# Kernel optimization log

Measured on AMD Instinct MI355X. Metric: run time of the kernel, lower is better.

The kernel has to match this reference:

```python
import jax, jax.numpy as jnp
import numpy as np

N_NODES = 50000
N_EDGES = 600000
N_GRAPHS = 500
NODES_PER_GRAPH = 100
D = 128


def gcn_conv(x, W, b, src, dst, norm, n_nodes):
    # x' = D^-1/2 (A+I) D^-1/2 (x @ W) + b   (PyG GCNConv, add_self_loops=True)
    xw = x @ W                                # [N, out]
    msg = xw[src] * norm[:, None]             # [E+N, out]
    out = jax.ops.segment_sum(msg, dst, num_segments=n_nodes)
    return out + b


def setup_inputs() -> dict:
    key = jax.random.key(0)
    ks = jax.random.split(key, 8)
    x = jax.random.normal(ks[0], (N_NODES, D), dtype=jnp.float32)
    edge_index = jax.random.randint(ks[1], (2, N_EDGES), 0, N_NODES, dtype=jnp.int64)
    # batch: 500 graphs of 100 nodes each
    batch = jnp.repeat(jnp.arange(N_GRAPHS, dtype=jnp.int64), NODES_PER_GRAPH)
    # exactly 2 neighbor nodes per graph (first two of each graph)
    pat = jnp.zeros((NODES_PER_GRAPH,), dtype=jnp.float32).at[:2].set(1.0)
    is_neighbor = jnp.tile(pat, N_GRAPHS)
    scale = 1.0 / np.sqrt(D)
    W1 = jax.random.normal(ks[2], (D, D), dtype=jnp.float32) * scale
    b1 = jnp.zeros((D,), dtype=jnp.float32)
    W2 = jax.random.normal(ks[3], (D, D), dtype=jnp.float32) * scale
    b2 = jnp.zeros((D,), dtype=jnp.float32)
    W3 = jax.random.normal(ks[4], (D, D), dtype=jnp.float32) * scale
    b3 = jnp.zeros((D,), dtype=jnp.float32)
    return {"x": x, "edge_index": edge_index, "is_neighbor": is_neighbor,
            "batch": batch, "W1": W1, "b1": b1, "W2": W2, "b2": b2,
            "W3": W3, "b3": b3}


def reference(x, edge_index, is_neighbor, batch, W1, b1, W2, b2, W3, b3):
    n = x.shape[0]
    loop = jnp.arange(n, dtype=edge_index.dtype)
    src = jnp.concatenate([edge_index[0], loop])   # self loops appended
    dst = jnp.concatenate([edge_index[1], loop])
    deg = jax.ops.segment_sum(jnp.ones_like(dst, dtype=x.dtype), dst, num_segments=n)
    dinv = jnp.where(deg > 0, jax.lax.rsqrt(deg), 0.0)
    norm = dinv[src] * dinv[dst]                   # [E+N]

    h = gcn_conv(x, W1, b1, src, dst, norm, n)
    h = jax.nn.relu(h)
    h = gcn_conv(h, W2, b2, src, dst, norm, n)
    h = jax.nn.relu(h)
    h = gcn_conv(h, W3, b3, src, dst, norm, n)

    h = h * is_neighbor[:, None]
    pooled = jax.ops.segment_sum(h, batch, num_segments=N_GRAPHS)
    return pooled / 2.0
```

## Files before the change

### kernel.cpp

```cpp
#include <hip/hip_runtime.h>
#include <hip/hip_fp16.h>
#include <type_traits>

#define D 128

typedef __attribute__((ext_vector_type(8))) _Float16 f16x8;
typedef __attribute__((ext_vector_type(4))) float f32x4;


__global__ void count_kernel(const int* __restrict__ src, const int* __restrict__ dst,
                             const float* __restrict__ is_n,
                             int* __restrict__ cnt, int* __restrict__ mark, int E) {
    int e = blockIdx.x * blockDim.x + threadIdx.x;
    if (e < E) {
        int d = dst[e];
        atomicAdd(&cnt[d], 1);
        if (is_n[d] != 0.f) mark[src[e]] = 1;
    }
}

__global__ __launch_bounds__(256) void psumB_kernel(const int* __restrict__ cnt,
                                                    const int* __restrict__ mark,
                                                    const float* __restrict__ is_n,
                                                    int* __restrict__ bsum_c,
                                                    int* __restrict__ bsum_m, int n) {
    __shared__ int s[256], s2[256];
    int t = threadIdx.x;
    int i = blockIdx.x * 256 + t;
    s[t] = (i < n) ? cnt[i] : 0;
    s2[t] = (i < n) ? (mark[i] | (is_n[i] != 0.f ? 1 : 0)) : 0;
    __syncthreads();
    for (int off = 128; off > 0; off >>= 1) {
        if (t < off) { s[t] += s[t + off]; s2[t] += s2[t + off]; }
        __syncthreads();
    }
    if (t == 0) { bsum_c[blockIdx.x] = s[0]; bsum_m[blockIdx.x] = s2[0]; }
}

__global__ __launch_bounds__(256) void bscanB_kernel(const int* __restrict__ bsum_c,
                                                     const int* __restrict__ bsum_m,
                                                     int* __restrict__ boff_c,
                                                     int* __restrict__ boff_m,
                                                     int* __restrict__ na, int PB) {
    __shared__ int s[256];
    int t = threadIdx.x;
    int v = (t < PB) ? bsum_c[t] : 0;
    s[t] = v;
    __syncthreads();
    for (int off = 1; off < 256; off <<= 1) {
        int add = (t >= off) ? s[t - off] : 0;
        __syncthreads();
        s[t] += add;
        __syncthreads();
    }
    if (t < PB) boff_c[t] = s[t] - v;
    __syncthreads();
    int v2 = (t < PB) ? bsum_m[t] : 0;
    s[t] = v2;
    __syncthreads();
    for (int off = 1; off < 256; off <<= 1) {
        int add = (t >= off) ? s[t - off] : 0;
        __syncthreads();
        s[t] += add;
        __syncthreads();
    }
    if (t < PB) boff_m[t] = s[t] - v2;
    if (t == PB - 1) na[0] = s[t];
}

__global__ __launch_bounds__(256) void finB_kernel(const int* __restrict__ cnt,
                                                   const int* __restrict__ mark,
                                                   const float* __restrict__ is_n,
                                                   const int* __restrict__ boff_c,
                                                   const int* __restrict__ boff_m,
                                                   int* __restrict__ rowstart,
                                                   int* __restrict__ cursor,
                                                   float* __restrict__ dinv,
                                                   int* __restrict__ act, int n, int E) {
    __shared__ int s[256];
    int t = threadIdx.x;
    int i = blockIdx.x * 256 + t;
    int c = (i < n) ? cnt[i] : 0;
    s[t] = c;
    __syncthreads();
    for (int off = 1; off < 256; off <<= 1) {
        int add = (t >= off) ? s[t - off] : 0;
        __syncthreads();
        s[t] += add;
        __syncthreads();
    }
    if (i < n) {
        int excl = s[t] - c + boff_c[blockIdx.x];
        rowstart[i] = excl;
        cursor[i] = excl;
        dinv[i] = rsqrtf(1.0f + (float)c);
    }
    if (i == 0) rowstart[n] = E;
    __syncthreads();
    int m = (i < n) ? (mark[i] | (is_n[i] != 0.f ? 1 : 0)) : 0;
    s[t] = m;
    __syncthreads();
    for (int off = 1; off < 256; off <<= 1) {
        int add = (t >= off) ? s[t - off] : 0;
        __syncthreads();
        s[t] += add;
        __syncthreads();
    }
    if (m) act[s[t] - 1 + boff_m[blockIdx.x]] = i;
}

__global__ void fill_kernel(const int* __restrict__ src, const int* __restrict__ dst,
                            int* __restrict__ cursor, int* __restrict__ csr_src, int E) {
    int e = blockIdx.x * blockDim.x + threadIdx.x;
    if (e < E) {
        int d = dst[e];
        int pos = atomicAdd(&cursor[d], 1);
        csr_src[pos] = src[e];
    }
}


__global__ __launch_bounds__(256) void packw_kernel(const float* __restrict__ W1,
                                                    const float* __restrict__ W2,
                                                    const float* __restrict__ W3,
                                                    __half* __restrict__ Wp) {
    int gid = blockIdx.x * 256 + threadIdx.x;
    int m = gid >> 11;
    int idx = gid & 2047;
    const float* W = (m == 0) ? W1 : (m == 1) ? W2 : W3;
    int l = idx & 63;
    int nt = (idx >> 6) & 7;
    int ks = idx >> 9;
    int kb = ks * 32 + (l >> 4) * 8;
    int col = nt * 16 + (l & 15);
    __half tmp[8];
#pragma unroll
    for (int j = 0; j < 8; j++) tmp[j] = __float2half(W[(kb + j) * D + col]);
    *(float4*)&Wp[(size_t)gid * 8] = *(float4*)tmp;
}


template <typename AT>
__global__ __launch_bounds__(256, 2) void gemm_mfma_kernel(const AT* __restrict__ X,
                                                           const __half* __restrict__ Wp,
                                                           const float* __restrict__ dinv,
                                                           __half* __restrict__ Y, int M) {
    int lane = threadIdx.x & 63;
    int wid = threadIdx.x >> 6;
    f16x8 bf[4][8];
    {
        const float4* wp = (const float4*)Wp;
#pragma unroll
        for (int ks = 0; ks < 4; ks++)
#pragma unroll
            for (int nt = 0; nt < 8; nt++) {
                float4 t = wp[(ks * 8 + nt) * 64 + lane];
                bf[ks][nt] = *(f16x8*)&t;
            }
    }
    int row_l = lane & 15;
    int kgrp = lane >> 4;
    int tiles = M >> 4;
    int nw = gridDim.x * 4;
    for (int tile = blockIdx.x * 4 + wid; tile < tiles; tile += nw) {
        int row0 = tile << 4;
        const AT* ap = X + (size_t)(row0 + row_l) * D + kgrp * 8;
        f32x4 acc[8];
#pragma unroll
        for (int nt = 0; nt < 8; nt++) acc[nt] = (f32x4){0.f, 0.f, 0.f, 0.f};
#pragma unroll
        for (int ks = 0; ks < 4; ks++) {
            f16x8 a;
            if constexpr (std::is_same<AT, float>::value) {
                float4 a0 = *(const float4*)(ap + ks * 32);
                float4 a1 = *(const float4*)(ap + ks * 32 + 4);
                a[0] = (_Float16)a0.x; a[1] = (_Float16)a0.y;
                a[2] = (_Float16)a0.z; a[3] = (_Float16)a0.w;
                a[4] = (_Float16)a1.x; a[5] = (_Float16)a1.y;
                a[6] = (_Float16)a1.z; a[7] = (_Float16)a1.w;
            } else {
                float4 t = *(const float4*)(const void*)(ap + ks * 32);
                a = *(f16x8*)&t;
            }
#pragma unroll
            for (int nt = 0; nt < 8; nt++)
                acc[nt] = __builtin_amdgcn_mfma_f32_16x16x32_f16(a, bf[ks][nt],
                                                                 acc[nt], 0, 0, 0);
        }
        float ds[4];
#pragma unroll
        for (int r = 0; r < 4; r++) ds[r] = dinv[row0 + kgrp * 4 + r];
        __half* yb = Y + (size_t)row0 * D;
#pragma unroll
        for (int nt = 0; nt < 8; nt++)
#pragma unroll
            for (int r = 0; r < 4; r++)
                yb[(size_t)(kgrp * 4 + r) * D + nt * 16 + row_l] =
                    __float2half(ds[r] * acc[nt][r]);
    }
}


__device__ __forceinline__ void add_row(float acc[8], const __half* __restrict__ XWs,
                                        int u, int l16) {
    float4 r = ((const float4*)(XWs + (size_t)u * D))[l16];
    const __half2* h2 = (const __half2*)&r;
#pragma unroll
    for (int k = 0; k < 4; k++) {
        float2 f = __half22float2(h2[k]);
        acc[2 * k]     += f.x;
        acc[2 * k + 1] += f.y;
    }
}

__device__ __forceinline__ void gather_grp(const __half* __restrict__ XWs,
                                           const int* __restrict__ csr_src,
                                           int v, int e0, int e1, int l16,
                                           float acc[8]) {
#pragma unroll
    for (int k = 0; k < 8; k++) acc[k] = 0.f;
    int j = e0;
    for (; j + 1 < e1; j += 2) {
        int u0 = csr_src[j];
        int u1 = csr_src[j + 1];
        float4 r0 = ((const float4*)(XWs + (size_t)u0 * D))[l16];
        float4 r1 = ((const float4*)(XWs + (size_t)u1 * D))[l16];
        const __half2* a0 = (const __half2*)&r0;
        const __half2* a1 = (const __half2*)&r1;
#pragma unroll
        for (int k = 0; k < 4; k++) {
            float2 f0 = __half22float2(a0[k]);
            float2 f1 = __half22float2(a1[k]);
            acc[2 * k]     += f0.x + f1.x;
            acc[2 * k + 1] += f0.y + f1.y;
        }
    }
    if (j < e1) add_row(acc, XWs, csr_src[j], l16);
    add_row(acc, XWs, v, l16);
}


__global__ __launch_bounds__(256) void agg_gemm_kernel(const __half* __restrict__ XWs,
                                                       const float* __restrict__ bias,
                                                       const float* __restrict__ dinv,
                                                       const int* __restrict__ rowstart,
                                                       const int* __restrict__ csr_src,
                                                       const __half* __restrict__ Wp2,
                                                       __half* __restrict__ Y) {
    __shared__ __half hs[16][136];
    int t = threadIdx.x;
    int wid = t >> 6, lane = t & 63;
    int g = lane >> 4, l16 = lane & 15;
    int block0 = blockIdx.x * 16;
    int v = block0 + wid * 4 + g;
    int e0 = rowstart[v], e1 = rowstart[v + 1];
    float acc[8];
    gather_grp(XWs, csr_src, v, e0, e1, l16, acc);
    float dv = dinv[v];
    float4 b0 = ((const float4*)bias)[l16 * 2];
    float4 b1 = ((const float4*)bias)[l16 * 2 + 1];
    __half o[8];
    o[0] = __float2half(fmaxf(b0.x + dv * acc[0], 0.f));
    o[1] = __float2half(fmaxf(b0.y + dv * acc[1], 0.f));
    o[2] = __float2half(fmaxf(b0.z + dv * acc[2], 0.f));
    o[3] = __float2half(fmaxf(b0.w + dv * acc[3], 0.f));
    o[4] = __float2half(fmaxf(b1.x + dv * acc[4], 0.f));
    o[5] = __float2half(fmaxf(b1.y + dv * acc[5], 0.f));
    o[6] = __float2half(fmaxf(b1.z + dv * acc[6], 0.f));
    o[7] = __float2half(fmaxf(b1.w + dv * acc[7], 0.f));
    *(float4*)&hs[wid * 4 + g][l16 * 8] = *(float4*)o;
    f16x8 bf[4][2];
    {
        const float4* wp = (const float4*)Wp2;
#pragma unroll
        for (int ks = 0; ks < 4; ks++)
#pragma unroll
            for (int j = 0; j < 2; j++) {
                float4 tmp = wp[(ks * 8 + wid * 2 + j) * 64 + lane];
                bf[ks][j] = *(f16x8*)&tmp;
            }
    }
    __syncthreads();
    int row_l = l16, kgrp = g;
    f32x4 acc2[2];
    acc2[0] = (f32x4){0.f, 0.f, 0.f, 0.f};
    acc2[1] = (f32x4){0.f, 0.f, 0.f, 0.f};
#pragma unroll
    for (int ks = 0; ks < 4; ks++) {
        f16x8 a = *(f16x8*)&hs[row_l][ks * 32 + kgrp * 8];
#pragma unroll
        for (int j = 0; j < 2; j++)
            acc2[j] = __builtin_amdgcn_mfma_f32_16x16x32_f16(a, bf[ks][j],
                                                             acc2[j], 0, 0, 0);
    }
    float ds[4];
#pragma unroll
    for (int r = 0; r < 4; r++) ds[r] = dinv[block0 + kgrp * 4 + r];
    __half* yb = Y + (size_t)block0 * D;
#pragma unroll
    for (int j = 0; j < 2; j++)
#pragma unroll
        for (int r = 0; r < 4; r++)
            yb[(size_t)(kgrp * 4 + r) * D + (wid * 2 + j) * 16 + row_l] =
                __float2half(ds[r] * acc2[j][r]);
}


__global__ __launch_bounds__(256) void agg_act_kernel(const __half* __restrict__ XWs,
                                                      const float* __restrict__ bias,
                                                      const float* __restrict__ dinv,
                                                      const int* __restrict__ rowstart,
                                                      const int* __restrict__ csr_src,
                                                      const int* __restrict__ act,
                                                      const int* __restrict__ na_p,
                                                      __half* __restrict__ out) {
    int t = threadIdx.x;
    int wid = t >> 6, lane = t & 63;
    int g = lane >> 4, l16 = lane & 15;
    int na = na_p[0];
    int stride = gridDim.x * 16;
    float4 b0 = ((const float4*)bias)[l16 * 2];
    float4 b1 = ((const float4*)bias)[l16 * 2 + 1];
    for (int i = blockIdx.x * 16 + wid * 4 + g; i < na; i += stride) {
        int v = act[i];
        int e0 = rowstart[v], e1 = rowstart[v + 1];
        float acc[8];
        gather_grp(XWs, csr_src, v, e0, e1, l16, acc);
        float dv = dinv[v];
        __half o[8];
        o[0] = __float2half(dv * fmaxf(b0.x + dv * acc[0], 0.f));
        o[1] = __float2half(dv * fmaxf(b0.y + dv * acc[1], 0.f));
        o[2] = __float2half(dv * fmaxf(b0.z + dv * acc[2], 0.f));
        o[3] = __float2half(dv * fmaxf(b0.w + dv * acc[3], 0.f));
        o[4] = __float2half(dv * fmaxf(b1.x + dv * acc[4], 0.f));
        o[5] = __float2half(dv * fmaxf(b1.y + dv * acc[5], 0.f));
        o[6] = __float2half(dv * fmaxf(b1.z + dv * acc[6], 0.f));
        o[7] = __float2half(dv * fmaxf(b1.w + dv * acc[7], 0.f));
        *(float4*)&out[(size_t)v * D + l16 * 8] = *(float4*)o;
    }
}


__global__ __launch_bounds__(256) void agg_pool_kernel(const __half* __restrict__ Hs,
                                                       const float* __restrict__ dinv,
                                                       const int* __restrict__ rowstart,
                                                       const int* __restrict__ csr_src,
                                                       const float* __restrict__ is_n,
                                                       const int* __restrict__ batch,
                                                       float* __restrict__ P,
                                                       float* __restrict__ cg, int n) {
    int t = threadIdx.x;
    int wid = t >> 6, lane = t & 63;
    int g = lane >> 4, l16 = lane & 15;
    int v = blockIdx.x * 16 + wid * 4 + g;
    float w_is = is_n[v];
    if (__ballot(w_is != 0.f) == 0ULL) return;
    if (w_is != 0.f) {
        int e0 = rowstart[v], e1 = rowstart[v + 1];
        float acc[8];
        gather_grp(Hs, csr_src, v, e0, e1, l16, acc);
        float s = w_is * dinv[v];
        int gr = batch[v];
        float* pb = &P[(size_t)gr * D + l16 * 8];
#pragma unroll
        for (int k = 0; k < 8; k++) atomicAdd(&pb[k], s * acc[k]);
        if (l16 == 0) atomicAdd(&cg[gr], w_is);
    }
}

__global__ __launch_bounds__(64) void pool_gemm_kernel(const float* __restrict__ P,
                                                       const float* __restrict__ cg,
                                                       const float* __restrict__ W,
                                                       const float* __restrict__ b,
                                                       float* __restrict__ out, int G) {
    int g = blockIdx.x;
    if (g >= G) return;
    int c = threadIdx.x * 2;
    float2 acc = {0.f, 0.f};
    const float* pr = &P[(size_t)g * D];
#pragma unroll 4
    for (int k = 0; k < D; k++) {
        float pk = pr[k];
        float2 w = *(const float2*)&W[k * D + c];
        acc.x += pk * w.x;
        acc.y += pk * w.y;
    }
    float s = 0.5f * cg[g];
    float2 bb = *(const float2*)&b[c];
    out[(size_t)g * D + c]     = 0.5f * acc.x + s * bb.x;
    out[(size_t)g * D + c + 1] = 0.5f * acc.y + s * bb.y;
}


extern "C" void kernel_launch(void* const* d_in, const int* in_sizes, int n_in,
                              void* d_out, int out_size, void* d_ws, size_t ws_size,
                              hipStream_t stream) {
    const float* x     = (const float*)d_in[0];
    const int*   edge  = (const int*)d_in[1];
    const float* is_n  = (const float*)d_in[2];
    const int*   batch = (const int*)d_in[3];
    const float* W1 = (const float*)d_in[4];
    const float* b1 = (const float*)d_in[5];
    const float* W2 = (const float*)d_in[6];
    const float* b2 = (const float*)d_in[7];
    const float* W3 = (const float*)d_in[8];
    const float* b3 = (const float*)d_in[9];
    float* out = (float*)d_out;

    int n = in_sizes[0] / D;
    int E = in_sizes[1] / 2;
    int G = out_size / D;
    const int* esrc = edge;
    const int* edst = edge + E;

    char* p = (char*)d_ws;
    __half* xw = (__half*)p;     p += (size_t)n * D * sizeof(float);
    __half* h  = (__half*)p;     p += (size_t)n * D * sizeof(float);
    float* dinv = (float*)p;     p += (size_t)n * sizeof(float);
    int* rowstart = (int*)p;     p += (size_t)(n + 1) * sizeof(int);
    int* cursor = (int*)p;       p += (size_t)n * sizeof(int);
    int* csr_src = (int*)p;      p += (size_t)E * sizeof(int);
    int* bsum_c = (int*)p;       p += 256 * sizeof(int);
    int* bsum_m = (int*)p;       p += 256 * sizeof(int);
    int* boff_c = (int*)p;       p += 256 * sizeof(int);
    int* boff_m = (int*)p;       p += 256 * sizeof(int);
    int* act = (int*)p;          p += (size_t)n * sizeof(int);
    int* na = (int*)p;           p += 4 * sizeof(int);
    __half* Wp = (__half*)p;     p += (size_t)3 * D * D * sizeof(__half);
    int* cnt = (int*)p;          p += (size_t)n * sizeof(int);
    int* mark = (int*)p;         p += (size_t)n * sizeof(int);
    float* P = (float*)p;        p += (size_t)G * D * sizeof(float);
    float* cg = (float*)p;       p += (size_t)G * sizeof(float);
    size_t zbytes = (size_t)(2 * n) * sizeof(int) + (size_t)(G * D + G) * sizeof(float);

    int PB = (n + 255) / 256;

    hipMemsetAsync(cnt, 0, zbytes, stream);
    packw_kernel<<<24, 256, 0, stream>>>(W1, W2, W3, Wp);
    count_kernel<<<(E + 255) / 256, 256, 0, stream>>>(esrc, edst, is_n, cnt, mark, E);
    psumB_kernel<<<PB, 256, 0, stream>>>(cnt, mark, is_n, bsum_c, bsum_m, n);
    bscanB_kernel<<<1, 256, 0, stream>>>(bsum_c, bsum_m, boff_c, boff_m, na, PB);
    finB_kernel<<<PB, 256, 0, stream>>>(cnt, mark, is_n, boff_c, boff_m,
                                        rowstart, cursor, dinv, act, n, E);
    fill_kernel<<<(E + 255) / 256, 256, 0, stream>>>(esrc, edst, cursor, csr_src, E);

    gemm_mfma_kernel<float><<<512, 256, 0, stream>>>(x, Wp, dinv, xw, n);
    agg_gemm_kernel<<<n / 16, 256, 0, stream>>>(xw, b1, dinv, rowstart, csr_src,
                                                Wp + D * D, h);
    agg_act_kernel<<<1024, 256, 0, stream>>>(h, b2, dinv, rowstart, csr_src, act, na, xw);
    agg_pool_kernel<<<n / 16, 256, 0, stream>>>(xw, dinv, rowstart, csr_src,
                                                is_n, batch, P, cg, n);
    pool_gemm_kernel<<<G, 64, 0, stream>>>(P, cg, W3, b3, out, G);
}
```

Baseline: 167.1 us.

## Pad CSR rows to multiples of four with zero-row sentinel and bitmask neighbor lookup

Rounds each destination's CSR segment up to a multiple of four and fills the padding with index n, which points at an extra zeroed row appended to the xw and h buffers. The gather loop can then load four indices at once with an int4 load and do four row fetches per iteration with no tail handling. It also packs is_neighbor into a bitmask that count_kernel reads instead of the float array. The cost is an extra pad kernel, more CSR storage, and wasted gathers of the zero row for the padding entries.

```diff
diff --git a/kernel.cpp b/kernel.cpp
--- a/kernel.cpp
+++ b/kernel.cpp
@@ -9,13 +9,13 @@
 
 
 __global__ void count_kernel(const int* __restrict__ src, const int* __restrict__ dst,
-                             const float* __restrict__ is_n,
+                             const unsigned int* __restrict__ bm,
                              int* __restrict__ cnt, int* __restrict__ mark, int E) {
     int e = blockIdx.x * blockDim.x + threadIdx.x;
     if (e < E) {
         int d = dst[e];
         atomicAdd(&cnt[d], 1);
-        if (is_n[d] != 0.f) mark[src[e]] = 1;
+        if ((bm[d >> 5] >> (d & 31)) & 1u) mark[src[e]] = 1;
     }
 }
 
@@ -27,7 +27,8 @@
     __shared__ int s[256], s2[256];
     int t = threadIdx.x;
     int i = blockIdx.x * 256 + t;
-    s[t] = (i < n) ? cnt[i] : 0;
+    int c = (i < n) ? cnt[i] : 0;
+    s[t] = (c + 3) & ~3;
     s2[t] = (i < n) ? (mark[i] | (is_n[i] != 0.f ? 1 : 0)) : 0;
     __syncthreads();
     for (int off = 128; off > 0; off >>= 1) {
@@ -54,6 +55,7 @@
         __syncthreads();
     }
     if (t < PB) boff_c[t] = s[t] - v;
+    if (t == PB - 1) na[1] = s[t];
     __syncthreads();
     int v2 = (t < PB) ? bsum_m[t] : 0;
     s[t] = v2;
@@ -73,15 +75,17 @@
                                                    const float* __restrict__ is_n,
                                                    const int* __restrict__ boff_c,
                                                    const int* __restrict__ boff_m,
+                                                   const int* __restrict__ na,
                                                    int* __restrict__ rowstart,
                                                    int* __restrict__ cursor,
                                                    float* __restrict__ dinv,
-                                                   int* __restrict__ act, int n, int E) {
+                                                   int* __restrict__ act, int n) {
     __shared__ int s[256];
     int t = threadIdx.x;
     int i = blockIdx.x * 256 + t;
     int c = (i < n) ? cnt[i] : 0;
-    s[t] = c;
+    int c4 = (c + 3) & ~3;
+    s[t] = c4;
     __syncthreads();
     for (int off = 1; off < 256; off <<= 1) {
         int add = (t >= off) ? s[t - off] : 0;
@@ -90,12 +94,12 @@
         __syncthreads();
     }
     if (i < n) {
-        int excl = s[t] - c + boff_c[blockIdx.x];
+        int excl = s[t] - c4 + boff_c[blockIdx.x];
         rowstart[i] = excl;
         cursor[i] = excl;
         dinv[i] = rsqrtf(1.0f + (float)c);
     }
-    if (i == 0) rowstart[n] = E;
+    if (i == 0) rowstart[n] = na[1];
     __syncthreads();
     int m = (i < n) ? (mark[i] | (is_n[i] != 0.f ? 1 : 0)) : 0;
     s[t] = m;
@@ -119,24 +123,58 @@
     }
 }
 
+__global__ void pad_kernel(const int* __restrict__ cursor,
+                           const int* __restrict__ rowstart,
+                           int* __restrict__ csr_src, int n) {
+    int v = blockIdx.x * blockDim.x + threadIdx.x;
+    if (v < n) {
+        int p = cursor[v], pe = rowstart[v + 1];
+        for (; p < pe; p++) csr_src[p] = n;
+    }
+}
+
 
 __global__ __launch_bounds__(256) void packw_kernel(const float* __restrict__ W1,
                                                     const float* __restrict__ W2,
                                                     const float* __restrict__ W3,
-                                                    __half* __restrict__ Wp) {
+                                                    __half* __restrict__ Wp,
+                                                    const float* __restrict__ is_n,
+                                                    unsigned int* __restrict__ bm,
+                                                    __half* __restrict__ xw,
+                                                    __half* __restrict__ h, int n) {
     int gid = blockIdx.x * 256 + threadIdx.x;
-    int m = gid >> 11;
-    int idx = gid & 2047;
-    const float* W = (m == 0) ? W1 : (m == 1) ? W2 : W3;
-    int l = idx & 63;
-    int nt = (idx >> 6) & 7;
-    int ks = idx >> 9;
-    int kb = ks * 32 + (l >> 4) * 8;
-    int col = nt * 16 + (l & 15);
-    __half tmp[8];
-#pragma unroll
-    for (int j = 0; j < 8; j++) tmp[j] = __float2half(W[(kb + j) * D + col]);
-    *(float4*)&Wp[(size_t)gid * 8] = *(float4*)tmp;
+    if (gid < 6144) {
+        int m = gid >> 11;
+        int idx = gid & 2047;
+        const float* W = (m == 0) ? W1 : (m == 1) ? W2 : W3;
+        int l = idx & 63;
+        int nt = (idx >> 6) & 7;
+        int ks = idx >> 9;
+        int kb = ks * 32 + (l >> 4) * 8;
+        int col = nt * 16 + (l & 15);
+        __half tmp[8];
+#pragma unroll
+        for (int j = 0; j < 8; j++) tmp[j] = __float2half(W[(kb + j) * D + col]);
+        *(float4*)&Wp[(size_t)gid * 8] = *(float4*)tmp;
+    } else if (gid < 6144 + 1563) {
+        int w = gid - 6144;
+        unsigned int bits = 0;
+        int base = w << 5;
+#pragma unroll 4
+        for (int k = 0; k < 32; k++) {
+            int i = base + k;
+            if (i < n && is_n[i] != 0.f) bits |= (1u << k);
+        }
+        bm[w] = bits;
+    } else if (gid < 6144 + 1563 + 16) {
+        int k = gid - (6144 + 1563);
+        float4 z = {0.f, 0.f, 0.f, 0.f};
+        *(float4*)&xw[(size_t)n * D + k * 8] = z;
+    } else if (gid < 6144 + 1563 + 32) {
+        int k = gid - (6144 + 1563 + 16);
+        float4 z = {0.f, 0.f, 0.f, 0.f};
+        *(float4*)&h[(size_t)n * D + k * 8] = z;
+    }
 }
 
 
@@ -201,42 +239,41 @@
 }
 
 
-__device__ __forceinline__ void add_row(float acc[8], const __half* __restrict__ XWs,
-                                        int u, int l16) {
-    float4 r = ((const float4*)(XWs + (size_t)u * D))[l16];
-    const __half2* h2 = (const __half2*)&r;
-#pragma unroll
-    for (int k = 0; k < 4; k++) {
-        float2 f = __half22float2(h2[k]);
-        acc[2 * k]     += f.x;
-        acc[2 * k + 1] += f.y;
-    }
-}
-
 __device__ __forceinline__ void gather_grp(const __half* __restrict__ XWs,
-                                           const int* __restrict__ csr_src,
+                                           const int* __restrict__ csr,
                                            int v, int e0, int e1, int l16,
                                            float acc[8]) {
+    float4 rs = ((const float4*)(XWs + (size_t)v * D))[l16];
 #pragma unroll
     for (int k = 0; k < 8; k++) acc[k] = 0.f;
-    int j = e0;
-    for (; j + 1 < e1; j += 2) {
-        int u0 = csr_src[j];
-        int u1 = csr_src[j + 1];
-        float4 r0 = ((const float4*)(XWs + (size_t)u0 * D))[l16];
-        float4 r1 = ((const float4*)(XWs + (size_t)u1 * D))[l16];
+#pragma unroll 2
+    for (int j = e0; j < e1; j += 4) {
+        int4 u = *(const int4*)&csr[j];
+        float4 r0 = ((const float4*)(XWs + (size_t)u.x * D))[l16];
+        float4 r1 = ((const float4*)(XWs + (size_t)u.y * D))[l16];
+        float4 r2 = ((const float4*)(XWs + (size_t)u.z * D))[l16];
+        float4 r3 = ((const float4*)(XWs + (size_t)u.w * D))[l16];
         const __half2* a0 = (const __half2*)&r0;
         const __half2* a1 = (const __half2*)&r1;
+        const __half2* a2 = (const __half2*)&r2;
+        const __half2* a3 = (const __half2*)&r3;
 #pragma unroll
         for (int k = 0; k < 4; k++) {
             float2 f0 = __half22float2(a0[k]);
             float2 f1 = __half22float2(a1[k]);
-            acc[2 * k]     += f0.x + f1.x;
-            acc[2 * k + 1] += f0.y + f1.y;
+            float2 f2 = __half22float2(a2[k]);
+            float2 f3 = __half22float2(a3[k]);
+            acc[2 * k]     += (f0.x + f1.x) + (f2.x + f3.x);
+            acc[2 * k + 1] += (f0.y + f1.y) + (f2.y + f3.y);
         }
     }
-    if (j < e1) add_row(acc, XWs, csr_src[j], l16);
-    add_row(acc, XWs, v, l16);
+    const __half2* as = (const __half2*)&rs;
+#pragma unroll
+    for (int k = 0; k < 4; k++) {
+        float2 f = __half22float2(as[k]);
+        acc[2 * k] += f.x;
+        acc[2 * k + 1] += f.y;
+    }
 }
 
 
@@ -419,7 +456,7 @@
     float* dinv = (float*)p;     p += (size_t)n * sizeof(float);
     int* rowstart = (int*)p;     p += (size_t)(n + 1) * sizeof(int);
     int* cursor = (int*)p;       p += (size_t)n * sizeof(int);
-    int* csr_src = (int*)p;      p += (size_t)E * sizeof(int);
+    int* csr_src = (int*)p;      p += ((size_t)E + 3 * n) * sizeof(int);
     int* bsum_c = (int*)p;       p += 256 * sizeof(int);
     int* bsum_m = (int*)p;       p += 256 * sizeof(int);
     int* boff_c = (int*)p;       p += 256 * sizeof(int);
@@ -427,6 +464,7 @@
     int* act = (int*)p;          p += (size_t)n * sizeof(int);
     int* na = (int*)p;           p += 4 * sizeof(int);
     __half* Wp = (__half*)p;     p += (size_t)3 * D * D * sizeof(__half);
+    unsigned int* bm = (unsigned int*)p; p += 1600 * sizeof(unsigned int);
     int* cnt = (int*)p;          p += (size_t)n * sizeof(int);
     int* mark = (int*)p;         p += (size_t)n * sizeof(int);
     float* P = (float*)p;        p += (size_t)G * D * sizeof(float);
@@ -436,13 +474,14 @@
     int PB = (n + 255) / 256;
 
     hipMemsetAsync(cnt, 0, zbytes, stream);
-    packw_kernel<<<24, 256, 0, stream>>>(W1, W2, W3, Wp);
-    count_kernel<<<(E + 255) / 256, 256, 0, stream>>>(esrc, edst, is_n, cnt, mark, E);
+    packw_kernel<<<31, 256, 0, stream>>>(W1, W2, W3, Wp, is_n, bm, xw, h, n);
+    count_kernel<<<(E + 255) / 256, 256, 0, stream>>>(esrc, edst, bm, cnt, mark, E);
     psumB_kernel<<<PB, 256, 0, stream>>>(cnt, mark, is_n, bsum_c, bsum_m, n);
     bscanB_kernel<<<1, 256, 0, stream>>>(bsum_c, bsum_m, boff_c, boff_m, na, PB);
-    finB_kernel<<<PB, 256, 0, stream>>>(cnt, mark, is_n, boff_c, boff_m,
-                                        rowstart, cursor, dinv, act, n, E);
+    finB_kernel<<<PB, 256, 0, stream>>>(cnt, mark, is_n, boff_c, boff_m, na,
+                                        rowstart, cursor, dinv, act, n);
     fill_kernel<<<(E + 255) / 256, 256, 0, stream>>>(esrc, edst, cursor, csr_src, E);
+    pad_kernel<<<PB, 256, 0, stream>>>(cursor, rowstart, csr_src, n);
 
     gemm_mfma_kernel<float><<<512, 256, 0, stream>>>(x, Wp, dinv, xw, n);
     agg_gemm_kernel<<<n / 16, 256, 0, stream>>>(xw, b1, dinv, rowstart, csr_src,
```

Result: no change. 166.6 us (-0.3%).
